# Kernel tuning notes

Measured on AMD Instinct MI355X. Metric: run time of the kernel, lower is better.

## Reference

```python
import jax, jax.numpy as jnp
import numpy as np

DIM = 64
N_ENTITY = 100000
N_RELATION = 32
N_LAYER = 2
B = 4096
T = 32


def setup_inputs() -> dict:
    key = jax.random.key(0)
    ks = jax.random.split(key, 16)
    inp = {
        'users': jax.random.randint(ks[0], (B,), 0, 50000),
        'items': jax.random.randint(ks[1], (B,), 0, 20000),
        'user_h': jax.random.randint(ks[2], (N_LAYER, B, T), 0, N_ENTITY),
        'user_r': jax.random.randint(ks[3], (N_LAYER, B, T), 0, N_RELATION),
        'user_t': jax.random.randint(ks[4], (N_LAYER, B, T), 0, N_ENTITY),
        'item_h': jax.random.randint(ks[5], (N_LAYER, B, T), 0, N_ENTITY),
        'item_r': jax.random.randint(ks[6], (N_LAYER, B, T), 0, N_RELATION),
        'item_t': jax.random.randint(ks[7], (N_LAYER, B, T), 0, N_ENTITY),
        # learned params (xavier-ish scale), stored [in, out] for clean matmuls
        'ent_emb': jax.random.normal(ks[8], (N_ENTITY, DIM), jnp.float32) * 0.05,
        'rel_emb': jax.random.normal(ks[9], (N_RELATION, DIM), jnp.float32) * 0.05,
        'att_w1': jax.random.normal(ks[10], (2 * DIM, DIM), jnp.float32) * 0.1,
        'att_w2': jax.random.normal(ks[11], (DIM, DIM), jnp.float32) * 0.1,
        'att_w3': jax.random.normal(ks[12], (DIM, 1), jnp.float32) * 0.1,
        'gate_w1': jax.random.normal(ks[13], (2 * DIM, DIM), jnp.float32) * 0.1,
        'gate_w2': jax.random.normal(ks[14], (DIM, DIM), jnp.float32) * 0.1,
    }
    return inp


def _knowledge_attention(h_e, r_e, t_e, att_w1, att_w2, att_w3, gate_w1, gate_w2):
    # h_e/r_e/t_e: [L, B, T, D]
    x = jnp.concatenate([h_e, r_e], axis=-1)                      # [L,B,T,2D]
    s = jax.nn.relu(jnp.einsum('lbtk,kd->lbtd', x, att_w1))
    s = jax.nn.relu(jnp.einsum('lbtd,de->lbte', s, att_w2))
    s = jax.nn.sigmoid(jnp.einsum('lbtd,do->lbto', s, att_w3))[..., 0]  # [L,B,T]
    att = jax.nn.softmax(s, axis=-1)                              # softmax over neighbors
    gate = 2.0 * jax.nn.sigmoid(
        jnp.einsum('lbtd,de->lbte',
                   jax.nn.relu(jnp.einsum('lbtk,kd->lbtd', x, gate_w1)),
                   gate_w2))                                       # [L,B,T,D]
    return jnp.sum(att[..., None] * gate * t_e, axis=2)          # [L,B,D]


def reference(users, items, user_h, user_r, user_t, item_h, item_r, item_t,
              ent_emb, rel_emb, att_w1, att_w2, att_w3, gate_w1, gate_w2):
    # ---- user tower ----
    u_h = ent_emb[user_h]   # [L,B,T,D]
    u_r = rel_emb[user_r]
    u_t = ent_emb[user_t]
    user_origin = jnp.mean(u_h[0], axis=1)                        # [B,D]
    u_layers = _knowledge_attention(u_h, u_r, u_t, att_w1, att_w2, att_w3,
                                    gate_w1, gate_w2)             # [L,B,D]
    e_u = jnp.concatenate([user_origin] + [u_layers[i] for i in range(N_LAYER)], axis=-1)
    # ---- item tower ----
    i_h = ent_emb[item_h]
    i_r = rel_emb[item_r]
    i_t = ent_emb[item_t]
    item_origin = ent_emb[items]                                  # [B,D]
    i_layers = _knowledge_attention(i_h, i_r, i_t, att_w1, att_w2, att_w3,
                                    gate_w1, gate_w2)
    e_v = jnp.concatenate([item_origin] + [i_layers[i] for i in range(N_LAYER)], axis=-1)
    # ---- predict (agg='concat', single concat block per tower) ----
    scores = jax.nn.sigmoid(jnp.sum(e_u * e_v, axis=1))           # [B]
    return scores
```

## Files before the change

### kernel.cpp

```cpp
#include <hip/hip_runtime.h>

#define DIM 64
#define NB 4096
#define NTOK 32
#define BPB 8

typedef __attribute__((ext_vector_type(8))) __bf16 bf16x8;
typedef __attribute__((ext_vector_type(4))) float f32x4;

__device__ __forceinline__ f32x4 mfma16(bf16x8 a, bf16x8 b, f32x4 c) {
  return __builtin_amdgcn_mfma_f32_16x16x32_bf16(a, b, c, 0, 0, 0);
}

#define SWC(row, col) ((col) ^ (((row) & 7) << 3))

__global__ void prep_w(const float* __restrict__ W1, const float* __restrict__ G1,
                       const float* __restrict__ W2, const float* __restrict__ G2,
                       __bf16* __restrict__ ws) {
  int i = blockIdx.x * 256 + threadIdx.x;
  if (i < 8192) {
    int c = i >> 7, k = i & 127;
    ws[i]        = (__bf16)W1[k * 64 + c];
    ws[8192 + i] = (__bf16)G1[k * 64 + c];
  } else if (i < 12288) {
    int j = i - 8192;
    int c = j >> 6, k = j & 63;
    ws[16384 + j] = (__bf16)W2[k * 64 + c];
    ws[20480 + j] = (__bf16)G2[k * 64 + c];
  }
}

__global__ __launch_bounds__(256) void ckan_fast(
    const int* __restrict__ items, const int* __restrict__ user_h,
    const int* __restrict__ user_r, const int* __restrict__ user_t,
    const int* __restrict__ item_h, const int* __restrict__ item_r,
    const int* __restrict__ item_t,
    const float* __restrict__ ent, const float* __restrict__ rel,
    const __bf16* __restrict__ wsb, const float* __restrict__ w3,
    float* __restrict__ out)
{
  __shared__ __align__(16) __bf16 buf[128][64];
  __shared__ float outbuf[BPB][4][64];
  __shared__ float pu_lds[BPB];

  const int tid  = threadIdx.x;
  const int w    = tid >> 6;
  const int lane = tid & 63;
  const int r16  = lane & 15;
  const int g4   = lane >> 4;
  const int rb   = w * 32;
  const int b0   = blockIdx.x * BPB;
  const int l    = w >> 1;
  const int tower = w & 1;

  const __bf16* __restrict__ W1t = wsb;
  const __bf16* __restrict__ G1t = wsb + 8192;
  const __bf16* __restrict__ W2t = wsb + 16384;
  const __bf16* __restrict__ G2t = wsb + 20480;

  const int* __restrict__ Hp = tower ? item_h : user_h;
  const int* __restrict__ Rp = tower ? item_r : user_r;
  const int* __restrict__ Tp = tower ? item_t : user_t;

  float w3c[4];
#pragma unroll
  for (int n = 0; n < 4; ++n) w3c[n] = w3[n * 16 + r16];

  const f32x4 zero4 = {0.f, 0.f, 0.f, 0.f};

  int ib = (l * NB + b0) * NTOK;
  int h0  = Hp[ib + r16] * DIM,      h1  = Hp[ib + 16 + r16] * DIM;
  int rr0 = Rp[ib + r16] * DIM,      rr1 = Rp[ib + 16 + r16] * DIM;
  int t0  = Tp[ib + r16] * DIM,      t1  = Tp[ib + 16 + r16] * DIM;
  int ioidx = items[b0] * DIM;

#pragma unroll 1
  for (int it = 0; it < BPB; ++it) {
    f32x4 axlo[4][2], axhi[4][2];
#pragma unroll
    for (int kk = 0; kk < 4; ++kk)
#pragma unroll
      for (int m = 0; m < 2; ++m) {
        const float* src = (kk < 2)
            ? ent + (m ? h1 : h0) + kk * 32 + g4 * 8
            : rel + (m ? rr1 : rr0) + (kk - 2) * 32 + g4 * 8;
        axlo[kk][m] = *(const f32x4*)(src);
        axhi[kk][m] = *(const f32x4*)(src + 4);
      }
    f32x4 io0l = zero4, io0h = zero4, io1l = zero4, io1h = zero4;
    if (w == 0) {
      io0l = *(const f32x4*)(ent + ioidx + g4 * 8);
      io0h = *(const f32x4*)(ent + ioidx + g4 * 8 + 4);
      io1l = *(const f32x4*)(ent + ioidx + 32 + g4 * 8);
      io1h = *(const f32x4*)(ent + ioidx + 32 + g4 * 8 + 4);
    }

    int h0n = h0, h1n = h1, rr0n = rr0, rr1n = rr1, t0n = t0, t1n = t1, ion = ioidx;
    if (it + 1 < BPB) {
      const int ibn = ib + NTOK;
      h0n  = Hp[ibn + r16] * DIM;      h1n  = Hp[ibn + 16 + r16] * DIM;
      rr0n = Rp[ibn + r16] * DIM;      rr1n = Rp[ibn + 16 + r16] * DIM;
      t0n  = Tp[ibn + r16] * DIM;      t1n  = Tp[ibn + 16 + r16] * DIM;
      ion  = items[b0 + it + 1] * DIM;
      ib = ibn;
    }

    float uo[2][8];
    if (w == 0) {
#pragma unroll
      for (int kk = 0; kk < 2; ++kk)
#pragma unroll
        for (int j = 0; j < 4; ++j) {
          uo[kk][j]     = axlo[kk][0][j] + axlo[kk][1][j];
          uo[kk][4 + j] = axhi[kk][0][j] + axhi[kk][1][j];
        }
    }

    bf16x8 afr[4][2];
#pragma unroll
    for (int kk = 0; kk < 4; ++kk)
#pragma unroll
      for (int m = 0; m < 2; ++m) {
        bf16x8 a;
#pragma unroll
        for (int j = 0; j < 4; ++j) {
          a[j]     = (__bf16)axlo[kk][m][j];
          a[4 + j] = (__bf16)axhi[kk][m][j];
        }
        afr[kk][m] = a;
      }

    f32x4 accS[2][4], accG[2][4];
#pragma unroll
    for (int m = 0; m < 2; ++m)
#pragma unroll
      for (int n = 0; n < 4; ++n) { accS[m][n] = zero4; accG[m][n] = zero4; }
#pragma unroll
    for (int kk = 0; kk < 4; ++kk)
#pragma unroll
      for (int n = 0; n < 4; ++n) {
        bf16x8 bS = *(const bf16x8*)(W1t + (n * 16 + r16) * 128 + kk * 32 + g4 * 8);
        bf16x8 bG = *(const bf16x8*)(G1t + (n * 16 + r16) * 128 + kk * 32 + g4 * 8);
#pragma unroll
        for (int m = 0; m < 2; ++m) {
          accS[m][n] = mfma16(afr[kk][m], bS, accS[m][n]);
          accG[m][n] = mfma16(afr[kk][m], bG, accG[m][n]);
        }
      }

    f32x4 telo[2][2], tehi[2][2];
#pragma unroll
    for (int m2 = 0; m2 < 2; ++m2)
#pragma unroll
      for (int h = 0; h < 2; ++h) {
        const float* ts = ent + (m2 ? t1 : t0) + h * 32 + g4 * 8;
        telo[m2][h] = *(const f32x4*)(ts);
        tehi[m2][h] = *(const f32x4*)(ts + 4);
      }

#pragma unroll
    for (int m = 0; m < 2; ++m)
#pragma unroll
      for (int n = 0; n < 4; ++n)
#pragma unroll
        for (int i = 0; i < 4; ++i) {
          const int row = rb + m * 16 + g4 * 4 + i;
          const int col = n * 16 + r16;
          buf[row][SWC(row, col)] = (__bf16)fmaxf(accS[m][n][i], 0.f);
        }

    f32x4 acc2S[2][4];
#pragma unroll
    for (int m = 0; m < 2; ++m)
#pragma unroll
      for (int n = 0; n < 4; ++n) acc2S[m][n] = zero4;
#pragma unroll
    for (int kk = 0; kk < 2; ++kk) {
      bf16x8 aS[2];
#pragma unroll
      for (int m = 0; m < 2; ++m) {
        const int tok = rb + m * 16 + r16;
        aS[m] = *(const bf16x8*)&buf[tok][SWC(tok, kk * 32 + g4 * 8)];
      }
#pragma unroll
      for (int n = 0; n < 4; ++n) {
        bf16x8 bS = *(const bf16x8*)(W2t + (n * 16 + r16) * 64 + kk * 32 + g4 * 8);
#pragma unroll
        for (int m = 0; m < 2; ++m) acc2S[m][n] = mfma16(aS[m], bS, acc2S[m][n]);
      }
    }

    float att[2][4];
    {
      float dotp[2][4];
#pragma unroll
      for (int m = 0; m < 2; ++m)
#pragma unroll
        for (int i = 0; i < 4; ++i) {
          float d = 0.f;
#pragma unroll
          for (int n = 0; n < 4; ++n)
            d += fmaxf(acc2S[m][n][i], 0.f) * w3c[n];
          dotp[m][i] = d;
        }
#pragma unroll
      for (int off = 1; off <= 8; off <<= 1)
#pragma unroll
        for (int m = 0; m < 2; ++m)
#pragma unroll
          for (int i = 0; i < 4; ++i)
            dotp[m][i] += __shfl_xor(dotp[m][i], off);
      float den = 0.f;
#pragma unroll
      for (int m = 0; m < 2; ++m)
#pragma unroll
        for (int i = 0; i < 4; ++i) {
          const float sc = 1.f / (1.f + __expf(-dotp[m][i]));
          att[m][i] = __expf(sc);
          den += att[m][i];
        }
      den += __shfl_xor(den, 16);
      den += __shfl_xor(den, 32);
      const float inv = 1.f / den;
#pragma unroll
      for (int m = 0; m < 2; ++m)
#pragma unroll
        for (int i = 0; i < 4; ++i) att[m][i] *= inv;
    }

#pragma unroll
    for (int m = 0; m < 2; ++m)
#pragma unroll
      for (int n = 0; n < 4; ++n)
#pragma unroll
        for (int i = 0; i < 4; ++i) {
          const int row = rb + m * 16 + g4 * 4 + i;
          const int col = n * 16 + r16;
          buf[row][SWC(row, col)] = (__bf16)fmaxf(accG[m][n][i], 0.f);
        }

    f32x4 acc2G[2][4];
#pragma unroll
    for (int m = 0; m < 2; ++m)
#pragma unroll
      for (int n = 0; n < 4; ++n) acc2G[m][n] = zero4;
#pragma unroll
    for (int kk = 0; kk < 2; ++kk) {
      bf16x8 aG[2];
#pragma unroll
      for (int m = 0; m < 2; ++m) {
        const int tok = rb + m * 16 + r16;
        aG[m] = *(const bf16x8*)&buf[tok][SWC(tok, kk * 32 + g4 * 8)];
      }
#pragma unroll
      for (int n = 0; n < 4; ++n) {
        bf16x8 bG = *(const bf16x8*)(G2t + (n * 16 + r16) * 64 + kk * 32 + g4 * 8);
#pragma unroll
        for (int m = 0; m < 2; ++m) acc2G[m][n] = mfma16(aG[m], bG, acc2G[m][n]);
      }
    }

#pragma unroll
    for (int m = 0; m < 2; ++m)
#pragma unroll
      for (int n = 0; n < 4; ++n)
#pragma unroll
        for (int i = 0; i < 4; ++i) {
          const int row = rb + m * 16 + g4 * 4 + i;
          const int col = n * 16 + r16;
          const float g2v = 2.f / (1.f + __expf(-acc2G[m][n][i]));
          buf[row][SWC(row, col)] = (__bf16)(att[m][i] * g2v);
        }

    float dsum[2][8];
#pragma unroll
    for (int h = 0; h < 2; ++h)
#pragma unroll
      for (int j = 0; j < 8; ++j) dsum[h][j] = 0.f;

#pragma unroll
    for (int m2 = 0; m2 < 2; ++m2) {
      const int prow = rb + m2 * 16 + r16;
#pragma unroll
      for (int h = 0; h < 2; ++h) {
        bf16x8 pf = *(const bf16x8*)&buf[prow][SWC(prow, h * 32 + g4 * 8)];
#pragma unroll
        for (int j = 0; j < 4; ++j) {
          dsum[h][j]     += (float)pf[j]     * telo[m2][h][j];
          dsum[h][4 + j] += (float)pf[4 + j] * tehi[m2][h][j];
        }
      }
    }
#pragma unroll
    for (int off = 1; off <= 8; off <<= 1)
#pragma unroll
      for (int h = 0; h < 2; ++h)
#pragma unroll
        for (int j = 0; j < 8; ++j)
          dsum[h][j] += __shfl_xor(dsum[h][j], off);
    if (r16 == 0) {
#pragma unroll
      for (int h = 0; h < 2; ++h)
#pragma unroll
        for (int j = 0; j < 8; ++j)
          outbuf[it][w][h * 32 + g4 * 8 + j] = dsum[h][j];
    }

    if (w == 0) {
      float s = 0.f;
#pragma unroll
      for (int j = 0; j < 4; ++j) {
        s += uo[0][j] * io0l[j] + uo[0][4 + j] * io0h[j];
        s += uo[1][j] * io1l[j] + uo[1][4 + j] * io1h[j];
      }
      s *= (1.f / 32.f);
#pragma unroll
      for (int off = 1; off <= 32; off <<= 1) s += __shfl_xor(s, off);
      if (lane == 0) pu_lds[it] = s;
    }

    h0 = h0n; h1 = h1n; rr0 = rr0n; rr1 = rr1n; t0 = t0n; t1 = t1n; ioidx = ion;
  }

  __syncthreads();

  if (w == 0) {
#pragma unroll 1
    for (int bb = 0; bb < BPB; ++bb) {
      float part = outbuf[bb][0][lane] * outbuf[bb][1][lane]
                 + outbuf[bb][2][lane] * outbuf[bb][3][lane];
#pragma unroll
      for (int off = 32; off >= 1; off >>= 1) part += __shfl_xor(part, off);
      if (lane == 0) out[b0 + bb] = 1.f / (1.f + __expf(-(part + pu_lds[bb])));
    }
  }
}

extern "C" void kernel_launch(void* const* d_in, const int* in_sizes, int n_in,
                              void* d_out, int out_size, void* d_ws, size_t ws_size,
                              hipStream_t stream) {
  const int*   items  = (const int*)d_in[1];
  const int*   user_h = (const int*)d_in[2];
  const int*   user_r = (const int*)d_in[3];
  const int*   user_t = (const int*)d_in[4];
  const int*   item_h = (const int*)d_in[5];
  const int*   item_r = (const int*)d_in[6];
  const int*   item_t = (const int*)d_in[7];
  const float* ent    = (const float*)d_in[8];
  const float* rel    = (const float*)d_in[9];
  const float* W1     = (const float*)d_in[10];
  const float* W2     = (const float*)d_in[11];
  const float* w3     = (const float*)d_in[12];
  const float* G1     = (const float*)d_in[13];
  const float* G2     = (const float*)d_in[14];
  __bf16* wsb = (__bf16*)d_ws;
  float* out = (float*)d_out;

  prep_w<<<dim3(48), dim3(256), 0, stream>>>(W1, G1, W2, G2, wsb);
  ckan_fast<<<dim3(NB / BPB), dim3(256), 0, stream>>>(
      items, user_h, user_r, user_t, item_h, item_r, item_t,
      ent, rel, wsb, w3, out);
}
```

Baseline: 142.6 us.

## Software-pipeline embedding gathers one batch element ahead of MFMA compute

Adds a prologue that gathers the first element's h/r embeddings and converts them to bf16 fragments. Inside the loop it then issues the next element's h/r/item gathers before the current element's MFMAs, and converts them after the attention and gate stages. The gate second layer is reordered ahead of the score path, and the user-origin dot product moves next to the prefetch. The aim is to hide global gather latency behind matrix work, at the cost of more live registers, which may reduce occupancy.

```diff
diff --git a/kernel.cpp b/kernel.cpp
--- a/kernel.cpp
+++ b/kernel.cpp
@@ -69,54 +69,31 @@
   const f32x4 zero4 = {0.f, 0.f, 0.f, 0.f};
 
   int ib = (l * NB + b0) * NTOK;
-  int h0  = Hp[ib + r16] * DIM,      h1  = Hp[ib + 16 + r16] * DIM;
-  int rr0 = Rp[ib + r16] * DIM,      rr1 = Rp[ib + 16 + r16] * DIM;
-  int t0  = Tp[ib + r16] * DIM,      t1  = Tp[ib + 16 + r16] * DIM;
-  int ioidx = items[b0] * DIM;
-
-#pragma unroll 1
-  for (int it = 0; it < BPB; ++it) {
-    f32x4 axlo[4][2], axhi[4][2];
+  int hn0 = Hp[ib + r16] * DIM,      hn1 = Hp[ib + 16 + r16] * DIM;
+  int rn0 = Rp[ib + r16] * DIM,      rn1 = Rp[ib + 16 + r16] * DIM;
+  int tn0 = Tp[ib + r16] * DIM,      tn1 = Tp[ib + 16 + r16] * DIM;
+  int ion = items[b0] * DIM;
+
+  bf16x8 afr[4][2];
+  {
+    f32x4 axlo[4][2], axhi[4][2], iol[2], ioh[2];
 #pragma unroll
     for (int kk = 0; kk < 4; ++kk)
 #pragma unroll
       for (int m = 0; m < 2; ++m) {
         const float* src = (kk < 2)
-            ? ent + (m ? h1 : h0) + kk * 32 + g4 * 8
-            : rel + (m ? rr1 : rr0) + (kk - 2) * 32 + g4 * 8;
+            ? ent + (m ? hn1 : hn0) + kk * 32 + g4 * 8
+            : rel + (m ? rn1 : rn0) + (kk - 2) * 32 + g4 * 8;
         axlo[kk][m] = *(const f32x4*)(src);
         axhi[kk][m] = *(const f32x4*)(src + 4);
       }
-    f32x4 io0l = zero4, io0h = zero4, io1l = zero4, io1h = zero4;
     if (w == 0) {
-      io0l = *(const f32x4*)(ent + ioidx + g4 * 8);
-      io0h = *(const f32x4*)(ent + ioidx + g4 * 8 + 4);
-      io1l = *(const f32x4*)(ent + ioidx + 32 + g4 * 8);
-      io1h = *(const f32x4*)(ent + ioidx + 32 + g4 * 8 + 4);
-    }
-
-    int h0n = h0, h1n = h1, rr0n = rr0, rr1n = rr1, t0n = t0, t1n = t1, ion = ioidx;
-    if (it + 1 < BPB) {
-      const int ibn = ib + NTOK;
-      h0n  = Hp[ibn + r16] * DIM;      h1n  = Hp[ibn + 16 + r16] * DIM;
-      rr0n = Rp[ibn + r16] * DIM;      rr1n = Rp[ibn + 16 + r16] * DIM;
-      t0n  = Tp[ibn + r16] * DIM;      t1n  = Tp[ibn + 16 + r16] * DIM;
-      ion  = items[b0 + it + 1] * DIM;
-      ib = ibn;
-    }
-
-    float uo[2][8];
-    if (w == 0) {
-#pragma unroll
-      for (int kk = 0; kk < 2; ++kk)
-#pragma unroll
-        for (int j = 0; j < 4; ++j) {
-          uo[kk][j]     = axlo[kk][0][j] + axlo[kk][1][j];
-          uo[kk][4 + j] = axhi[kk][0][j] + axhi[kk][1][j];
-        }
-    }
-
-    bf16x8 afr[4][2];
+#pragma unroll
+      for (int h = 0; h < 2; ++h) {
+        iol[h] = *(const f32x4*)(ent + ion + h * 32 + g4 * 8);
+        ioh[h] = *(const f32x4*)(ent + ion + h * 32 + g4 * 8 + 4);
+      }
+    }
 #pragma unroll
     for (int kk = 0; kk < 4; ++kk)
 #pragma unroll
@@ -129,6 +106,61 @@
         }
         afr[kk][m] = a;
       }
+    if (w == 0) {
+      float s = 0.f;
+#pragma unroll
+      for (int j = 0; j < 4; ++j) {
+        s += (axlo[0][0][j] + axlo[0][1][j]) * iol[0][j]
+           + (axhi[0][0][j] + axhi[0][1][j]) * ioh[0][j]
+           + (axlo[1][0][j] + axlo[1][1][j]) * iol[1][j]
+           + (axhi[1][0][j] + axhi[1][1][j]) * ioh[1][j];
+      }
+      s *= (1.f / 32.f);
+#pragma unroll
+      for (int off = 1; off <= 32; off <<= 1) s += __shfl_xor(s, off);
+      if (lane == 0) pu_lds[0] = s;
+    }
+  }
+  int tc0 = tn0, tc1 = tn1;
+  ib += NTOK;
+  hn0 = Hp[ib + r16] * DIM;  hn1 = Hp[ib + 16 + r16] * DIM;
+  rn0 = Rp[ib + r16] * DIM;  rn1 = Rp[ib + 16 + r16] * DIM;
+  tn0 = Tp[ib + r16] * DIM;  tn1 = Tp[ib + 16 + r16] * DIM;
+  ion = items[b0 + 1] * DIM;
+
+#pragma unroll 1
+  for (int it = 0; it < BPB; ++it) {
+    const bool more = (it + 1 < BPB);
+
+    f32x4 telo[2][2], tehi[2][2];
+#pragma unroll
+    for (int m2 = 0; m2 < 2; ++m2)
+#pragma unroll
+      for (int h = 0; h < 2; ++h) {
+        const float* ts = ent + (m2 ? tc1 : tc0) + h * 32 + g4 * 8;
+        telo[m2][h] = *(const f32x4*)(ts);
+        tehi[m2][h] = *(const f32x4*)(ts + 4);
+      }
+    f32x4 axlo[4][2], axhi[4][2], iol[2], ioh[2];
+    if (more) {
+#pragma unroll
+      for (int kk = 0; kk < 4; ++kk)
+#pragma unroll
+        for (int m = 0; m < 2; ++m) {
+          const float* src = (kk < 2)
+              ? ent + (m ? hn1 : hn0) + kk * 32 + g4 * 8
+              : rel + (m ? rn1 : rn0) + (kk - 2) * 32 + g4 * 8;
+          axlo[kk][m] = *(const f32x4*)(src);
+          axhi[kk][m] = *(const f32x4*)(src + 4);
+        }
+      if (w == 0) {
+#pragma unroll
+        for (int h = 0; h < 2; ++h) {
+          iol[h] = *(const f32x4*)(ent + ion + h * 32 + g4 * 8);
+          ioh[h] = *(const f32x4*)(ent + ion + h * 32 + g4 * 8 + 4);
+        }
+      }
+    }
 
     f32x4 accS[2][4], accG[2][4];
 #pragma unroll
@@ -148,15 +180,36 @@
         }
       }
 
-    f32x4 telo[2][2], tehi[2][2];
-#pragma unroll
-    for (int m2 = 0; m2 < 2; ++m2)
-#pragma unroll
-      for (int h = 0; h < 2; ++h) {
-        const float* ts = ent + (m2 ? t1 : t0) + h * 32 + g4 * 8;
-        telo[m2][h] = *(const f32x4*)(ts);
-        tehi[m2][h] = *(const f32x4*)(ts + 4);
-      }
+#pragma unroll
+    for (int m = 0; m < 2; ++m)
+#pragma unroll
+      for (int n = 0; n < 4; ++n)
+#pragma unroll
+        for (int i = 0; i < 4; ++i) {
+          const int row = rb + m * 16 + g4 * 4 + i;
+          const int col = n * 16 + r16;
+          buf[row][SWC(row, col)] = (__bf16)fmaxf(accG[m][n][i], 0.f);
+        }
+    f32x4 acc2G[2][4];
+#pragma unroll
+    for (int m = 0; m < 2; ++m)
+#pragma unroll
+      for (int n = 0; n < 4; ++n) acc2G[m][n] = zero4;
+#pragma unroll
+    for (int kk = 0; kk < 2; ++kk) {
+      bf16x8 aG[2];
+#pragma unroll
+      for (int m = 0; m < 2; ++m) {
+        const int tok = rb + m * 16 + r16;
+        aG[m] = *(const bf16x8*)&buf[tok][SWC(tok, kk * 32 + g4 * 8)];
+      }
+#pragma unroll
+      for (int n = 0; n < 4; ++n) {
+        bf16x8 bG = *(const bf16x8*)(G2t + (n * 16 + r16) * 64 + kk * 32 + g4 * 8);
+#pragma unroll
+        for (int m = 0; m < 2; ++m) acc2G[m][n] = mfma16(aG[m], bG, acc2G[m][n]);
+      }
+    }
 
 #pragma unroll
     for (int m = 0; m < 2; ++m)
@@ -168,7 +221,6 @@
           const int col = n * 16 + r16;
           buf[row][SWC(row, col)] = (__bf16)fmaxf(accS[m][n][i], 0.f);
         }
-
     f32x4 acc2S[2][4];
 #pragma unroll
     for (int m = 0; m < 2; ++m)
@@ -228,35 +280,40 @@
         for (int i = 0; i < 4; ++i) att[m][i] *= inv;
     }
 
-#pragma unroll
-    for (int m = 0; m < 2; ++m)
-#pragma unroll
-      for (int n = 0; n < 4; ++n)
-#pragma unroll
-        for (int i = 0; i < 4; ++i) {
-          const int row = rb + m * 16 + g4 * 4 + i;
-          const int col = n * 16 + r16;
-          buf[row][SWC(row, col)] = (__bf16)fmaxf(accG[m][n][i], 0.f);
-        }
-
-    f32x4 acc2G[2][4];
-#pragma unroll
-    for (int m = 0; m < 2; ++m)
-#pragma unroll
-      for (int n = 0; n < 4; ++n) acc2G[m][n] = zero4;
-#pragma unroll
-    for (int kk = 0; kk < 2; ++kk) {
-      bf16x8 aG[2];
-#pragma unroll
-      for (int m = 0; m < 2; ++m) {
-        const int tok = rb + m * 16 + r16;
-        aG[m] = *(const bf16x8*)&buf[tok][SWC(tok, kk * 32 + g4 * 8)];
-      }
-#pragma unroll
-      for (int n = 0; n < 4; ++n) {
-        bf16x8 bG = *(const bf16x8*)(G2t + (n * 16 + r16) * 64 + kk * 32 + g4 * 8);
-#pragma unroll
-        for (int m = 0; m < 2; ++m) acc2G[m][n] = mfma16(aG[m], bG, acc2G[m][n]);
+    if (more) {
+#pragma unroll
+      for (int kk = 0; kk < 4; ++kk)
+#pragma unroll
+        for (int m = 0; m < 2; ++m) {
+          bf16x8 a;
+#pragma unroll
+          for (int j = 0; j < 4; ++j) {
+            a[j]     = (__bf16)axlo[kk][m][j];
+            a[4 + j] = (__bf16)axhi[kk][m][j];
+          }
+          afr[kk][m] = a;
+        }
+      if (w == 0) {
+        float s = 0.f;
+#pragma unroll
+        for (int j = 0; j < 4; ++j) {
+          s += (axlo[0][0][j] + axlo[0][1][j]) * iol[0][j]
+             + (axhi[0][0][j] + axhi[0][1][j]) * ioh[0][j]
+             + (axlo[1][0][j] + axlo[1][1][j]) * iol[1][j]
+             + (axhi[1][0][j] + axhi[1][1][j]) * ioh[1][j];
+        }
+        s *= (1.f / 32.f);
+#pragma unroll
+        for (int off = 1; off <= 32; off <<= 1) s += __shfl_xor(s, off);
+        if (lane == 0) pu_lds[it + 1] = s;
+      }
+      tc0 = tn0; tc1 = tn1;
+      if (it + 2 < BPB) {
+        ib += NTOK;
+        hn0 = Hp[ib + r16] * DIM;  hn1 = Hp[ib + 16 + r16] * DIM;
+        rn0 = Rp[ib + r16] * DIM;  rn1 = Rp[ib + 16 + r16] * DIM;
+        tn0 = Tp[ib + r16] * DIM;  tn1 = Tp[ib + 16 + r16] * DIM;
+        ion = items[b0 + it + 2] * DIM;
       }
     }
 
@@ -277,7 +334,6 @@
     for (int h = 0; h < 2; ++h)
 #pragma unroll
       for (int j = 0; j < 8; ++j) dsum[h][j] = 0.f;
-
 #pragma unroll
     for (int m2 = 0; m2 < 2; ++m2) {
       const int prow = rb + m2 * 16 + r16;
@@ -305,21 +361,6 @@
         for (int j = 0; j < 8; ++j)
           outbuf[it][w][h * 32 + g4 * 8 + j] = dsum[h][j];
     }
-
-    if (w == 0) {
-      float s = 0.f;
-#pragma unroll
-      for (int j = 0; j < 4; ++j) {
-        s += uo[0][j] * io0l[j] + uo[0][4 + j] * io0h[j];
-        s += uo[1][j] * io1l[j] + uo[1][4 + j] * io1h[j];
-      }
-      s *= (1.f / 32.f);
-#pragma unroll
-      for (int off = 1; off <= 32; off <<= 1) s += __shfl_xor(s, off);
-      if (lane == 0) pu_lds[it] = s;
-    }
-
-    h0 = h0n; h1 = h1n; rr0 = rr0n; rr1 = rr1n; t0 = t0n; t1 = t1n; ioidx = ion;
   }
 
   __syncthreads();
```

Result: slower. 158.5 us (+11.1%).

## Swap MFMA operand order to produce transposed tiles and fuse gate epilogue in registers

Applied to the files above, without the earlier changes.

The MFMA operands are swapped so each lane holds four consecutive feature columns of one token (transposed output). That allows vectorized bf16x4 LDS writes into a padded per-wave buffer instead of scalar swizzled stores. Because the attention weight and t-embedding are now already in the same register layout, the final gate×attention×tail product is computed in registers, removing one LDS round trip and the read-back pass. The attention dot reduction changes from shuffles over 16 lanes per element to two cross-group shuffles.

```diff
diff --git a/kernel.cpp b/kernel.cpp
--- a/kernel.cpp
+++ b/kernel.cpp
@@ -6,13 +6,12 @@
 #define BPB 8
 
 typedef __attribute__((ext_vector_type(8))) __bf16 bf16x8;
+typedef __attribute__((ext_vector_type(4))) __bf16 bf16x4;
 typedef __attribute__((ext_vector_type(4))) float f32x4;
 
 __device__ __forceinline__ f32x4 mfma16(bf16x8 a, bf16x8 b, f32x4 c) {
   return __builtin_amdgcn_mfma_f32_16x16x32_bf16(a, b, c, 0, 0, 0);
 }
-
-#define SWC(row, col) ((col) ^ (((row) & 7) << 3))
 
 __global__ void prep_w(const float* __restrict__ W1, const float* __restrict__ G1,
                        const float* __restrict__ W2, const float* __restrict__ G2,
@@ -39,7 +38,7 @@
     const __bf16* __restrict__ wsb, const float* __restrict__ w3,
     float* __restrict__ out)
 {
-  __shared__ __align__(16) __bf16 buf[128][64];
+  __shared__ __align__(16) __bf16 buf[4][32][72];
   __shared__ float outbuf[BPB][4][64];
   __shared__ float pu_lds[BPB];
 
@@ -48,7 +47,6 @@
   const int lane = tid & 63;
   const int r16  = lane & 15;
   const int g4   = lane >> 4;
-  const int rb   = w * 32;
   const int b0   = blockIdx.x * BPB;
   const int l    = w >> 1;
   const int tower = w & 1;
@@ -62,17 +60,18 @@
   const int* __restrict__ Rp = tower ? item_r : user_r;
   const int* __restrict__ Tp = tower ? item_t : user_t;
 
-  float w3c[4];
-#pragma unroll
-  for (int n = 0; n < 4; ++n) w3c[n] = w3[n * 16 + r16];
+  f32x4 w3v[4];
+#pragma unroll
+  for (int n2 = 0; n2 < 4; ++n2)
+    w3v[n2] = *(const f32x4*)(w3 + n2 * 16 + g4 * 4);
 
   const f32x4 zero4 = {0.f, 0.f, 0.f, 0.f};
 
   int ib = (l * NB + b0) * NTOK;
-  int h0  = Hp[ib + r16] * DIM,      h1  = Hp[ib + 16 + r16] * DIM;
-  int rr0 = Rp[ib + r16] * DIM,      rr1 = Rp[ib + 16 + r16] * DIM;
-  int t0  = Tp[ib + r16] * DIM,      t1  = Tp[ib + 16 + r16] * DIM;
-  int ioidx = items[b0] * DIM;
+  int h0  = Hp[ib + r16] * DIM,   h1  = Hp[ib + 16 + r16] * DIM;
+  int rr0 = Rp[ib + r16] * DIM,   rr1 = Rp[ib + 16 + r16] * DIM;
+  int t0  = Tp[ib + r16] * DIM,   t1  = Tp[ib + 16 + r16] * DIM;
+  int ion = items[b0] * DIM;
 
 #pragma unroll 1
   for (int it = 0; it < BPB; ++it) {
@@ -80,238 +79,40 @@
 #pragma unroll
     for (int kk = 0; kk < 4; ++kk)
 #pragma unroll
-      for (int m = 0; m < 2; ++m) {
+      for (int m2 = 0; m2 < 2; ++m2) {
         const float* src = (kk < 2)
-            ? ent + (m ? h1 : h0) + kk * 32 + g4 * 8
-            : rel + (m ? rr1 : rr0) + (kk - 2) * 32 + g4 * 8;
-        axlo[kk][m] = *(const f32x4*)(src);
-        axhi[kk][m] = *(const f32x4*)(src + 4);
-      }
-    f32x4 io0l = zero4, io0h = zero4, io1l = zero4, io1h = zero4;
+            ? ent + (m2 ? h1 : h0) + kk * 32 + g4 * 8
+            : rel + (m2 ? rr1 : rr0) + (kk - 2) * 32 + g4 * 8;
+        axlo[kk][m2] = *(const f32x4*)(src);
+        axhi[kk][m2] = *(const f32x4*)(src + 4);
+      }
+    f32x4 iol[2], ioh[2];
     if (w == 0) {
-      io0l = *(const f32x4*)(ent + ioidx + g4 * 8);
-      io0h = *(const f32x4*)(ent + ioidx + g4 * 8 + 4);
-      io1l = *(const f32x4*)(ent + ioidx + 32 + g4 * 8);
-      io1h = *(const f32x4*)(ent + ioidx + 32 + g4 * 8 + 4);
-    }
-
-    int h0n = h0, h1n = h1, rr0n = rr0, rr1n = rr1, t0n = t0, t1n = t1, ion = ioidx;
+#pragma unroll
+      for (int h = 0; h < 2; ++h) {
+        iol[h] = *(const f32x4*)(ent + ion + h * 32 + g4 * 8);
+        ioh[h] = *(const f32x4*)(ent + ion + h * 32 + g4 * 8 + 4);
+      }
+    }
+
+    int h0n = h0, h1n = h1, rr0n = rr0, rr1n = rr1, t0n = t0, t1n = t1, ionn = ion;
     if (it + 1 < BPB) {
       const int ibn = ib + NTOK;
-      h0n  = Hp[ibn + r16] * DIM;      h1n  = Hp[ibn + 16 + r16] * DIM;
-      rr0n = Rp[ibn + r16] * DIM;      rr1n = Rp[ibn + 16 + r16] * DIM;
-      t0n  = Tp[ibn + r16] * DIM;      t1n  = Tp[ibn + 16 + r16] * DIM;
-      ion  = items[b0 + it + 1] * DIM;
+      h0n  = Hp[ibn + r16] * DIM;   h1n  = Hp[ibn + 16 + r16] * DIM;
+      rr0n = Rp[ibn + r16] * DIM;   rr1n = Rp[ibn + 16 + r16] * DIM;
+      t0n  = Tp[ibn + r16] * DIM;   t1n  = Tp[ibn + 16 + r16] * DIM;
+      ionn = items[b0 + it + 1] * DIM;
       ib = ibn;
-    }
-
-    float uo[2][8];
-    if (w == 0) {
-#pragma unroll
-      for (int kk = 0; kk < 2; ++kk)
-#pragma unroll
-        for (int j = 0; j < 4; ++j) {
-          uo[kk][j]     = axlo[kk][0][j] + axlo[kk][1][j];
-          uo[kk][4 + j] = axhi[kk][0][j] + axhi[kk][1][j];
-        }
-    }
-
-    bf16x8 afr[4][2];
-#pragma unroll
-    for (int kk = 0; kk < 4; ++kk)
-#pragma unroll
-      for (int m = 0; m < 2; ++m) {
-        bf16x8 a;
-#pragma unroll
-        for (int j = 0; j < 4; ++j) {
-          a[j]     = (__bf16)axlo[kk][m][j];
-          a[4 + j] = (__bf16)axhi[kk][m][j];
-        }
-        afr[kk][m] = a;
-      }
-
-    f32x4 accS[2][4], accG[2][4];
-#pragma unroll
-    for (int m = 0; m < 2; ++m)
-#pragma unroll
-      for (int n = 0; n < 4; ++n) { accS[m][n] = zero4; accG[m][n] = zero4; }
-#pragma unroll
-    for (int kk = 0; kk < 4; ++kk)
-#pragma unroll
-      for (int n = 0; n < 4; ++n) {
-        bf16x8 bS = *(const bf16x8*)(W1t + (n * 16 + r16) * 128 + kk * 32 + g4 * 8);
-        bf16x8 bG = *(const bf16x8*)(G1t + (n * 16 + r16) * 128 + kk * 32 + g4 * 8);
-#pragma unroll
-        for (int m = 0; m < 2; ++m) {
-          accS[m][n] = mfma16(afr[kk][m], bS, accS[m][n]);
-          accG[m][n] = mfma16(afr[kk][m], bG, accG[m][n]);
-        }
-      }
-
-    f32x4 telo[2][2], tehi[2][2];
-#pragma unroll
-    for (int m2 = 0; m2 < 2; ++m2)
-#pragma unroll
-      for (int h = 0; h < 2; ++h) {
-        const float* ts = ent + (m2 ? t1 : t0) + h * 32 + g4 * 8;
-        telo[m2][h] = *(const f32x4*)(ts);
-        tehi[m2][h] = *(const f32x4*)(ts + 4);
-      }
-
-#pragma unroll
-    for (int m = 0; m < 2; ++m)
-#pragma unroll
-      for (int n = 0; n < 4; ++n)
-#pragma unroll
-        for (int i = 0; i < 4; ++i) {
-          const int row = rb + m * 16 + g4 * 4 + i;
-          const int col = n * 16 + r16;
-          buf[row][SWC(row, col)] = (__bf16)fmaxf(accS[m][n][i], 0.f);
-        }
-
-    f32x4 acc2S[2][4];
-#pragma unroll
-    for (int m = 0; m < 2; ++m)
-#pragma unroll
-      for (int n = 0; n < 4; ++n) acc2S[m][n] = zero4;
-#pragma unroll
-    for (int kk = 0; kk < 2; ++kk) {
-      bf16x8 aS[2];
-#pragma unroll
-      for (int m = 0; m < 2; ++m) {
-        const int tok = rb + m * 16 + r16;
-        aS[m] = *(const bf16x8*)&buf[tok][SWC(tok, kk * 32 + g4 * 8)];
-      }
-#pragma unroll
-      for (int n = 0; n < 4; ++n) {
-        bf16x8 bS = *(const bf16x8*)(W2t + (n * 16 + r16) * 64 + kk * 32 + g4 * 8);
-#pragma unroll
-        for (int m = 0; m < 2; ++m) acc2S[m][n] = mfma16(aS[m], bS, acc2S[m][n]);
-      }
-    }
-
-    float att[2][4];
-    {
-      float dotp[2][4];
-#pragma unroll
-      for (int m = 0; m < 2; ++m)
-#pragma unroll
-        for (int i = 0; i < 4; ++i) {
-          float d = 0.f;
-#pragma unroll
-          for (int n = 0; n < 4; ++n)
-            d += fmaxf(acc2S[m][n][i], 0.f) * w3c[n];
-          dotp[m][i] = d;
-        }
-#pragma unroll
-      for (int off = 1; off <= 8; off <<= 1)
-#pragma unroll
-        for (int m = 0; m < 2; ++m)
-#pragma unroll
-          for (int i = 0; i < 4; ++i)
-            dotp[m][i] += __shfl_xor(dotp[m][i], off);
-      float den = 0.f;
-#pragma unroll
-      for (int m = 0; m < 2; ++m)
-#pragma unroll
-        for (int i = 0; i < 4; ++i) {
-          const float sc = 1.f / (1.f + __expf(-dotp[m][i]));
-          att[m][i] = __expf(sc);
-          den += att[m][i];
-        }
-      den += __shfl_xor(den, 16);
-      den += __shfl_xor(den, 32);
-      const float inv = 1.f / den;
-#pragma unroll
-      for (int m = 0; m < 2; ++m)
-#pragma unroll
-        for (int i = 0; i < 4; ++i) att[m][i] *= inv;
-    }
-
-#pragma unroll
-    for (int m = 0; m < 2; ++m)
-#pragma unroll
-      for (int n = 0; n < 4; ++n)
-#pragma unroll
-        for (int i = 0; i < 4; ++i) {
-          const int row = rb + m * 16 + g4 * 4 + i;
-          const int col = n * 16 + r16;
-          buf[row][SWC(row, col)] = (__bf16)fmaxf(accG[m][n][i], 0.f);
-        }
-
-    f32x4 acc2G[2][4];
-#pragma unroll
-    for (int m = 0; m < 2; ++m)
-#pragma unroll
-      for (int n = 0; n < 4; ++n) acc2G[m][n] = zero4;
-#pragma unroll
-    for (int kk = 0; kk < 2; ++kk) {
-      bf16x8 aG[2];
-#pragma unroll
-      for (int m = 0; m < 2; ++m) {
-        const int tok = rb + m * 16 + r16;
-        aG[m] = *(const bf16x8*)&buf[tok][SWC(tok, kk * 32 + g4 * 8)];
-      }
-#pragma unroll
-      for (int n = 0; n < 4; ++n) {
-        bf16x8 bG = *(const bf16x8*)(G2t + (n * 16 + r16) * 64 + kk * 32 + g4 * 8);
-#pragma unroll
-        for (int m = 0; m < 2; ++m) acc2G[m][n] = mfma16(aG[m], bG, acc2G[m][n]);
-      }
-    }
-
-#pragma unroll
-    for (int m = 0; m < 2; ++m)
-#pragma unroll
-      for (int n = 0; n < 4; ++n)
-#pragma unroll
-        for (int i = 0; i < 4; ++i) {
-          const int row = rb + m * 16 + g4 * 4 + i;
-          const int col = n * 16 + r16;
-          const float g2v = 2.f / (1.f + __expf(-acc2G[m][n][i]));
-          buf[row][SWC(row, col)] = (__bf16)(att[m][i] * g2v);
-        }
-
-    float dsum[2][8];
-#pragma unroll
-    for (int h = 0; h < 2; ++h)
-#pragma unroll
-      for (int j = 0; j < 8; ++j) dsum[h][j] = 0.f;
-
-#pragma unroll
-    for (int m2 = 0; m2 < 2; ++m2) {
-      const int prow = rb + m2 * 16 + r16;
-#pragma unroll
-      for (int h = 0; h < 2; ++h) {
-        bf16x8 pf = *(const bf16x8*)&buf[prow][SWC(prow, h * 32 + g4 * 8)];
-#pragma unroll
-        for (int j = 0; j < 4; ++j) {
-          dsum[h][j]     += (float)pf[j]     * telo[m2][h][j];
-          dsum[h][4 + j] += (float)pf[4 + j] * tehi[m2][h][j];
-        }
-      }
-    }
-#pragma unroll
-    for (int off = 1; off <= 8; off <<= 1)
-#pragma unroll
-      for (int h = 0; h < 2; ++h)
-#pragma unroll
-        for (int j = 0; j < 8; ++j)
-          dsum[h][j] += __shfl_xor(dsum[h][j], off);
-    if (r16 == 0) {
-#pragma unroll
-      for (int h = 0; h < 2; ++h)
-#pragma unroll
-        for (int j = 0; j < 8; ++j)
-          outbuf[it][w][h * 32 + g4 * 8 + j] = dsum[h][j];
     }
 
     if (w == 0) {
       float s = 0.f;
 #pragma unroll
       for (int j = 0; j < 4; ++j) {
-        s += uo[0][j] * io0l[j] + uo[0][4 + j] * io0h[j];
-        s += uo[1][j] * io1l[j] + uo[1][4 + j] * io1h[j];
+        s += (axlo[0][0][j] + axlo[0][1][j]) * iol[0][j]
+           + (axhi[0][0][j] + axhi[0][1][j]) * ioh[0][j]
+           + (axlo[1][0][j] + axlo[1][1][j]) * iol[1][j]
+           + (axhi[1][0][j] + axhi[1][1][j]) * ioh[1][j];
       }
       s *= (1.f / 32.f);
 #pragma unroll
@@ -319,7 +120,158 @@
       if (lane == 0) pu_lds[it] = s;
     }
 
-    h0 = h0n; h1 = h1n; rr0 = rr0n; rr1 = rr1n; t0 = t0n; t1 = t1n; ioidx = ion;
+    bf16x8 bfr[4][2];
+#pragma unroll
+    for (int kk = 0; kk < 4; ++kk)
+#pragma unroll
+      for (int m2 = 0; m2 < 2; ++m2) {
+        bf16x8 a;
+#pragma unroll
+        for (int j = 0; j < 4; ++j) {
+          a[j]     = (__bf16)axlo[kk][m2][j];
+          a[4 + j] = (__bf16)axhi[kk][m2][j];
+        }
+        bfr[kk][m2] = a;
+      }
+
+    f32x4 a1S[2][4], a1G[2][4];
+#pragma unroll
+    for (int m2 = 0; m2 < 2; ++m2)
+#pragma unroll
+      for (int n = 0; n < 4; ++n) { a1S[m2][n] = zero4; a1G[m2][n] = zero4; }
+#pragma unroll
+    for (int kk = 0; kk < 4; ++kk)
+#pragma unroll
+      for (int n = 0; n < 4; ++n) {
+        bf16x8 wS = *(const bf16x8*)(W1t + (n * 16 + r16) * 128 + kk * 32 + g4 * 8);
+        bf16x8 wG = *(const bf16x8*)(G1t + (n * 16 + r16) * 128 + kk * 32 + g4 * 8);
+#pragma unroll
+        for (int m2 = 0; m2 < 2; ++m2) {
+          a1S[m2][n] = mfma16(wS, bfr[kk][m2], a1S[m2][n]);
+          a1G[m2][n] = mfma16(wG, bfr[kk][m2], a1G[m2][n]);
+        }
+      }
+
+    f32x4 te[2][4];
+#pragma unroll
+    for (int m2 = 0; m2 < 2; ++m2)
+#pragma unroll
+      for (int n2 = 0; n2 < 4; ++n2)
+        te[m2][n2] = *(const f32x4*)(ent + (m2 ? t1 : t0) + n2 * 16 + g4 * 4);
+
+#pragma unroll
+    for (int m2 = 0; m2 < 2; ++m2)
+#pragma unroll
+      for (int n = 0; n < 4; ++n) {
+        bf16x4 v;
+#pragma unroll
+        for (int i = 0; i < 4; ++i) v[i] = (__bf16)fmaxf(a1S[m2][n][i], 0.f);
+        *(bf16x4*)&buf[w][m2 * 16 + r16][n * 16 + g4 * 4] = v;
+      }
+
+    f32x4 a2S[2][4];
+#pragma unroll
+    for (int m2 = 0; m2 < 2; ++m2)
+#pragma unroll
+      for (int n2 = 0; n2 < 4; ++n2) a2S[m2][n2] = zero4;
+#pragma unroll
+    for (int kk2 = 0; kk2 < 2; ++kk2) {
+      bf16x8 sf[2];
+#pragma unroll
+      for (int m2 = 0; m2 < 2; ++m2)
+        sf[m2] = *(const bf16x8*)&buf[w][m2 * 16 + r16][kk2 * 32 + g4 * 8];
+#pragma unroll
+      for (int n2 = 0; n2 < 4; ++n2) {
+        bf16x8 wS2 = *(const bf16x8*)(W2t + (n2 * 16 + r16) * 64 + kk2 * 32 + g4 * 8);
+#pragma unroll
+        for (int m2 = 0; m2 < 2; ++m2)
+          a2S[m2][n2] = mfma16(wS2, sf[m2], a2S[m2][n2]);
+      }
+    }
+
+    float att2[2];
+    {
+      float d0[2] = {0.f, 0.f};
+#pragma unroll
+      for (int m2 = 0; m2 < 2; ++m2)
+#pragma unroll
+        for (int n2 = 0; n2 < 4; ++n2)
+#pragma unroll
+          for (int i = 0; i < 4; ++i)
+            d0[m2] += fmaxf(a2S[m2][n2][i], 0.f) * w3v[n2][i];
+#pragma unroll
+      for (int m2 = 0; m2 < 2; ++m2) {
+        d0[m2] += __shfl_xor(d0[m2], 16);
+        d0[m2] += __shfl_xor(d0[m2], 32);
+        const float sc = 1.f / (1.f + __expf(-d0[m2]));
+        att2[m2] = __expf(sc);
+      }
+      float den = att2[0] + att2[1];
+#pragma unroll
+      for (int off = 1; off <= 8; off <<= 1) den += __shfl_xor(den, off);
+      const float inv = 1.f / den;
+      att2[0] *= inv; att2[1] *= inv;
+    }
+
+#pragma unroll
+    for (int m2 = 0; m2 < 2; ++m2)
+#pragma unroll
+      for (int n = 0; n < 4; ++n) {
+        bf16x4 v;
+#pragma unroll
+        for (int i = 0; i < 4; ++i) v[i] = (__bf16)fmaxf(a1G[m2][n][i], 0.f);
+        *(bf16x4*)&buf[w][m2 * 16 + r16][n * 16 + g4 * 4] = v;
+      }
+    f32x4 a2G[2][4];
+#pragma unroll
+    for (int m2 = 0; m2 < 2; ++m2)
+#pragma unroll
+      for (int n2 = 0; n2 < 4; ++n2) a2G[m2][n2] = zero4;
+#pragma unroll
+    for (int kk2 = 0; kk2 < 2; ++kk2) {
+      bf16x8 gf[2];
+#pragma unroll
+      for (int m2 = 0; m2 < 2; ++m2)
+        gf[m2] = *(const bf16x8*)&buf[w][m2 * 16 + r16][kk2 * 32 + g4 * 8];
+#pragma unroll
+      for (int n2 = 0; n2 < 4; ++n2) {
+        bf16x8 wG2 = *(const bf16x8*)(G2t + (n2 * 16 + r16) * 64 + kk2 * 32 + g4 * 8);
+#pragma unroll
+        for (int m2 = 0; m2 < 2; ++m2)
+          a2G[m2][n2] = mfma16(wG2, gf[m2], a2G[m2][n2]);
+      }
+    }
+
+    float dsum[4][4];
+#pragma unroll
+    for (int n2 = 0; n2 < 4; ++n2)
+#pragma unroll
+      for (int i = 0; i < 4; ++i) dsum[n2][i] = 0.f;
+#pragma unroll
+    for (int m2 = 0; m2 < 2; ++m2)
+#pragma unroll
+      for (int n2 = 0; n2 < 4; ++n2)
+#pragma unroll
+        for (int i = 0; i < 4; ++i) {
+          const float g2v = 2.f / (1.f + __expf(-a2G[m2][n2][i]));
+          dsum[n2][i] += att2[m2] * g2v * te[m2][n2][i];
+        }
+#pragma unroll
+    for (int off = 1; off <= 8; off <<= 1)
+#pragma unroll
+      for (int n2 = 0; n2 < 4; ++n2)
+#pragma unroll
+        for (int i = 0; i < 4; ++i)
+          dsum[n2][i] += __shfl_xor(dsum[n2][i], off);
+    if (r16 == 0) {
+#pragma unroll
+      for (int n2 = 0; n2 < 4; ++n2)
+#pragma unroll
+        for (int i = 0; i < 4; ++i)
+          outbuf[it][w][n2 * 16 + g4 * 4 + i] = dsum[n2][i];
+    }
+
+    h0 = h0n; h1 = h1n; rr0 = rr0n; rr1 = rr1n; t0 = t0n; t1 = t1n; ion = ionn;
   }
 
   __syncthreads();
```

After: 128.0 us. 1.11x faster.
